# Kernel tuning notes

Hardware: AMD Instinct MI355X
Metric: run time of the kernel (lower is better)

Reference implementation:

```python
import jax, jax.numpy as jnp
import numpy as np
from jax import lax

B, C, H, W = 32, 684, 16, 64
HID, A, CK, K = 256, 512, 512, 11


def setup_inputs() -> dict:
    key = jax.random.key(0)
    ks = jax.random.split(key, 12)
    s = 0.02
    return {
        "cnn_features": jax.random.normal(ks[0], (B, C, H, W), jnp.float32),
        "hidden": jax.random.normal(ks[1], (B, HID), jnp.float32),
        "alpha_sum": jax.random.uniform(ks[2], (B, 1, H, W), jnp.float32),
        "image_mask": jnp.ones((B, 1, H, W), jnp.float32),
        # hidden_weight: Linear(HID -> A)
        "Wh": jax.random.normal(ks[3], (A, HID), jnp.float32) * s,
        "bh": jnp.zeros((A,), jnp.float32),
        # encoder_feature_conv: Conv2d(C -> A, 1x1) == pointwise linear
        "Wec": jax.random.normal(ks[4], (A, C), jnp.float32) * s,
        "bec": jnp.zeros((A,), jnp.float32),
        # attention_conv: Conv2d(1 -> CK, 11x11, pad 5, no bias)
        "Wac": jax.random.normal(ks[5], (CK, 1, K, K), jnp.float32) * s,
        # attention_weight: Linear(CK -> A, no bias)
        "Waw": jax.random.normal(ks[6], (A, CK), jnp.float32) * s,
        # alpha_convert: Linear(A -> 1)
        "Wv": jax.random.normal(ks[7], (1, A), jnp.float32) * s,
        "bv": jnp.zeros((1,), jnp.float32),
    }


def reference(cnn_features, hidden, alpha_sum, image_mask,
              Wh, bh, Wec, bec, Wac, Waw, Wv, bv):
    # query = hidden_weight(hidden): [B, A]
    query = hidden @ Wh.T + bh
    # attention_conv(alpha_sum): [B, CK, H, W]
    ast = lax.conv_general_dilated(
        alpha_sum, Wac, window_strides=(1, 1),
        padding=[(K // 2, K // 2), (K // 2, K // 2)],
        dimension_numbers=("NCHW", "OIHW", "NCHW"))
    # attention_weight on permuted conv output: [B, H, W, A]
    coverage_alpha = jnp.einsum("bkhw,ak->bhwa", ast, Waw)
    # encoder_feature_conv (1x1 conv == pointwise linear): [B, H, W, A]
    cnn_trans = jnp.einsum("bchw,ac->bhwa", cnn_features, Wec) + bec
    # additive attention score
    alpha_score = jnp.tanh(query[:, None, None, :] + coverage_alpha + cnn_trans)
    # alpha_convert -> scalar energy per position: [B, H, W]
    energy = jnp.einsum("bhwa,a->bhw", alpha_score, Wv[0]) + bv[0]
    energy = energy - energy.max()  # global max-subtract as in original
    energy_exp = jnp.exp(energy) * image_mask[:, 0]
    denom = energy_exp.sum(axis=(-1, -2))[:, None, None] + 1e-10
    alpha = energy_exp / denom  # [B, H, W]
    alpha_sum_new = alpha[:, None, :, :] + alpha_sum  # [B, 1, H, W]
    # context: weighted spatial sum over features -> [B, C]
    context_vector = jnp.einsum("bhw,bchw->bc", alpha, cnn_features)
    return (context_vector, alpha, alpha_sum_new)
```

## Files before the change

kernel.cpp:

```cpp
#include <hip/hip_runtime.h>
#include <hip/hip_bf16.h>
#include <math.h>

#define Bn   32
#define Cn   684
#define Hn   16
#define Wn   64
#define HWn  1024
#define HIDn 256
#define An   512
#define KKn  121
#define CREAL 805
#define CPAD 832
#define NSTEP 26
#define NBLK 256

#define OUT_ALPHA 21888
#define OUT_ASUM  (21888 + 32768)

typedef short short8 __attribute__((ext_vector_type(8)));
typedef float floatx4 __attribute__((ext_vector_type(4)));

__device__ __forceinline__ unsigned short f2bf(float f) {
    union { float f; unsigned int i; } v; v.f = f;
    unsigned int i = v.i;
    return (unsigned short)((i + 0x7fffu + ((i >> 16) & 1u)) >> 16);
}
__device__ __forceinline__ unsigned int cvt2(float lo, float hi) {
    __hip_bfloat162 h = __float22bfloat162_rn(float2{lo, hi});
    union { __hip_bfloat162 h; unsigned int u; } cv; cv.h = h;
    return cv.u;
}

__device__ __forceinline__ size_t bfr_idx(int n, int k) {
    return ((((size_t)(n >> 4) * 26 + (k >> 5)) * 64
             + ((k >> 3) & 3) * 16 + (n & 15)) * 8) + (k & 7);
}

__global__ __launch_bounds__(256) void k_prep(
    const float* __restrict__ hidden,
    const float* __restrict__ Wh,
    const float* __restrict__ bh,
    const float* __restrict__ bec,
    const float* __restrict__ Wec,
    const float* __restrict__ Wac,
    const float* __restrict__ Waw,
    float* __restrict__ query,
    unsigned short* __restrict__ Bfr)
{
    __shared__ float sbuf[512];
    const int blk = blockIdx.x, t = threadIdx.x;
    if (blk < 512) {
        const int a = blk;
        sbuf[t]       = Waw[(size_t)a * 512 + t];
        sbuf[t + 256] = Waw[(size_t)a * 512 + t + 256];
        __syncthreads();
        for (int cp = t; cp < Cn; cp += 256)
            Bfr[bfr_idx(a, cp)] = f2bf(Wec[(size_t)a * Cn + cp]);
        if (t < KKn) {
            float s = 0.f;
            #pragma unroll 8
            for (int k = 0; k < 512; ++k)
                s = fmaf(sbuf[k], Wac[k * KKn + t], s);
            Bfr[bfr_idx(a, Cn + t)] = f2bf(s);
        }
        for (int cp = CREAL + t; cp < CPAD; cp += 256)
            Bfr[bfr_idx(a, cp)] = 0;
    } else {
        const int b = blk - 512;
        sbuf[t] = (t < HIDn) ? hidden[b * HIDn + t] : 0.f;
        __syncthreads();
        for (int a = t; a < An; a += 256) {
            const float4* wp = (const float4*)(Wh + (size_t)a * HIDn);
            float s = bh[a] + bec[a];
            #pragma unroll 8
            for (int i = 0; i < HIDn / 4; ++i) {
                float4 w = wp[i];
                s = fmaf(sbuf[4 * i],     w.x, s);
                s = fmaf(sbuf[4 * i + 1], w.y, s);
                s = fmaf(sbuf[4 * i + 2], w.z, s);
                s = fmaf(sbuf[4 * i + 3], w.w, s);
            }
            query[b * An + a] = s;
        }
    }
}

__device__ __forceinline__ float fetchU(const float* __restrict__ X,
                                        const float* plane,
                                        int m, int row) {
    if (row < Cn)   return X[(size_t)row * HWn + m];
    if (row < CREAL) {
        int ij = row - Cn; int di = ij / 11, dj = ij - di * 11;
        return plane[di * 74 + m + dj];
    }
    return 0.f;
}

__global__ __launch_bounds__(256, 4) void k_energy(
    const float* __restrict__ X,
    const float* __restrict__ asum,
    const float* __restrict__ Wv,
    const float* __restrict__ query,
    const unsigned short* __restrict__ Bfr,
    float* __restrict__ energy)
{
    __shared__ __align__(16) unsigned short As[2][64 * 40];
    __shared__ float plane[11 * 74 + 2];
    __shared__ float qs[NBLK];
    __shared__ float wvs[NBLK];
    __shared__ float red[4][64];

    const int t = threadIdx.x;
    const int d = blockIdx.x;
    const int nh  = (d >> 3) & 1;
    const int pid = (d >> 4) * 8 + (d & 7);
    const int hh = pid & 15, b = pid >> 4;
    const int w = t >> 6, lane = t & 63;
    const int q = lane >> 4, r = lane & 15;
    const int nbase = nh * NBLK;
    const int mA = t & 63;
    const int koA = t >> 6;

    const float* Xb = X + (size_t)b * Cn * HWn + hh * Wn;
    const unsigned short* Bp = Bfr + (size_t)(nh * 16 + w * 4) * 26 * 512;

    for (int i = t; i < 11 * 74; i += 256) {
        int di = i / 74, cc = i - di * 74;
        int h2 = hh + di - 5, w2 = cc - 5;
        float v = 0.f;
        if (h2 >= 0 && h2 < Hn && w2 >= 0 && w2 < Wn)
            v = asum[b * HWn + h2 * Wn + w2];
        plane[i] = v;
    }
    qs[t]  = query[b * An + nbase + t];
    wvs[t] = Wv[nbase + t];
    {
        const float* xp = Xb + (size_t)(koA * 8) * HWn + mA;
        uint4 u;
        u.x = cvt2(xp[0],              xp[(size_t)1 * HWn]);
        u.y = cvt2(xp[(size_t)2 * HWn], xp[(size_t)3 * HWn]);
        u.z = cvt2(xp[(size_t)4 * HWn], xp[(size_t)5 * HWn]);
        u.w = cvt2(xp[(size_t)6 * HWn], xp[(size_t)7 * HWn]);
        *(uint4*)&As[0][mA * 40 + koA * 8] = u;
    }
    __syncthreads();

    floatx4 acc[4][4];
    #pragma unroll
    for (int mf = 0; mf < 4; ++mf)
        #pragma unroll
        for (int nf = 0; nf < 4; ++nf)
            acc[mf][nf] = (floatx4){0.f, 0.f, 0.f, 0.f};

    for (int ch = 0; ch < NSTEP; ++ch) {
        const int cur = ch & 1;

        short8 bf[4];
        #pragma unroll
        for (int nf = 0; nf < 4; ++nf)
            bf[nf] = *(const short8*)(Bp + ((size_t)(nf * 26 + ch)) * 512 + lane * 8);

        short8 af[4];
        #pragma unroll
        for (int mf = 0; mf < 4; ++mf)
            af[mf] = *(const short8*)&As[cur][(mf * 16 + r) * 40 + q * 8];

        if (ch < NSTEP - 1) {
            const int c0 = (ch + 1) * 32 + koA * 8;
            float va[8];
            if (c0 + 7 < Cn) {
                const float* xp = Xb + (size_t)c0 * HWn + mA;
                #pragma unroll
                for (int j = 0; j < 8; ++j)
                    va[j] = xp[(size_t)j * HWn];
            } else {
                #pragma unroll
                for (int j = 0; j < 8; ++j)
                    va[j] = fetchU(Xb, plane, mA, c0 + j);
            }
            uint4 u;
            u.x = cvt2(va[0], va[1]);
            u.y = cvt2(va[2], va[3]);
            u.z = cvt2(va[4], va[5]);
            u.w = cvt2(va[6], va[7]);
            *(uint4*)&As[cur ^ 1][mA * 40 + koA * 8] = u;
        }

        #pragma unroll
        for (int mf = 0; mf < 4; ++mf)
            #pragma unroll
            for (int nf = 0; nf < 4; ++nf)
                acc[mf][nf] = __builtin_amdgcn_mfma_f32_16x16x32_bf16(
                    af[mf], bf[nf], acc[mf][nf], 0, 0, 0);

        __syncthreads();
    }

    float ep[16];
    #pragma unroll
    for (int i = 0; i < 16; ++i) ep[i] = 0.f;
    #pragma unroll
    for (int nf = 0; nf < 4; ++nf) {
        int nl = w * 64 + nf * 16 + r;
        float qv = qs[nl], wv = wvs[nl];
        #pragma unroll
        for (int mf = 0; mf < 4; ++mf)
            #pragma unroll
            for (int rg = 0; rg < 4; ++rg) {
                float x = acc[mf][nf][rg] + qv;
                float e2 = __expf(2.f * x);
                float th = 1.f - 2.f * __builtin_amdgcn_rcpf(e2 + 1.f);
                ep[mf * 4 + rg] += wv * th;
            }
    }
    #pragma unroll
    for (int i = 0; i < 16; ++i) {
        #pragma unroll
        for (int msk = 1; msk <= 8; msk <<= 1)
            ep[i] += __shfl_xor(ep[i], msk, 64);
    }
    if (r == 0) {
        #pragma unroll
        for (int mf = 0; mf < 4; ++mf)
            #pragma unroll
            for (int rg = 0; rg < 4; ++rg)
                red[w][mf * 16 + q * 4 + rg] = ep[mf * 4 + rg];
    }
    __syncthreads();
    if (t < 64) {
        float s = red[0][t] + red[1][t] + red[2][t] + red[3][t];
        atomicAdd(&energy[b * HWn + hh * Wn + t], s);
    }
}

__global__ __launch_bounds__(256) void k_softmax(
    const float* __restrict__ mask,
    const float* __restrict__ asum,
    float* __restrict__ energy,
    float* __restrict__ out)
{
    __shared__ float rsm[8];
    const int b = blockIdx.x;
    const int t = threadIdx.x, lane = t & 63, wid = t >> 6;

    float e[4], ex[4];
    #pragma unroll
    for (int i = 0; i < 4; ++i) e[i] = energy[b * HWn + i * 256 + t];
    float m = fmaxf(fmaxf(e[0], e[1]), fmaxf(e[2], e[3]));
    for (int off = 32; off >= 1; off >>= 1) m = fmaxf(m, __shfl_down(m, off, 64));
    if (lane == 0) rsm[wid] = m;
    __syncthreads();
    if (t == 0)
        rsm[4] = fmaxf(fmaxf(rsm[0], rsm[1]), fmaxf(rsm[2], rsm[3]));
    __syncthreads();
    const float M = rsm[4];
    float s = 0.f;
    #pragma unroll
    for (int i = 0; i < 4; ++i) {
        ex[i] = expf(e[i] - M) * mask[b * HWn + i * 256 + t];
        s += ex[i];
    }
    for (int off = 32; off >= 1; off >>= 1) s += __shfl_down(s, off, 64);
    __syncthreads();
    if (lane == 0) rsm[wid] = s;
    __syncthreads();
    if (t == 0) rsm[5] = rsm[0] + rsm[1] + rsm[2] + rsm[3] + 1e-10f;
    __syncthreads();
    const float denom = rsm[5];
    #pragma unroll
    for (int i = 0; i < 4; ++i) {
        int p = i * 256 + t;
        float a = ex[i] / denom;
        energy[b * HWn + p] = a;
        out[OUT_ALPHA + b * HWn + p] = a;
        out[OUT_ASUM  + b * HWn + p] = a + asum[b * HWn + p];
    }
}

__global__ __launch_bounds__(256) void k_ctx(
    const float* __restrict__ X,
    const float* __restrict__ alpha,
    float* __restrict__ out)
{
    __shared__ float al[1024];
    const int bx = blockIdx.x, b = blockIdx.y;
    const int t = threadIdx.x, lane = t & 63, wid = t >> 6;

    #pragma unroll
    for (int i = 0; i < 4; ++i) al[i * 256 + t] = alpha[b * HWn + i * 256 + t];
    __syncthreads();

    const int c = bx * 4 + wid;
    const float* xp = X + ((size_t)(b * Cn + c)) * HWn;
    float s2 = 0.f;
    #pragma unroll
    for (int i = 0; i < 4; ++i) {
        int off = i * 256 + lane * 4;
        float4 x = *(const float4*)(xp + off);
        float4 a = *(const float4*)(al + off);
        s2 = fmaf(a.x, x.x, s2);
        s2 = fmaf(a.y, x.y, s2);
        s2 = fmaf(a.z, x.z, s2);
        s2 = fmaf(a.w, x.w, s2);
    }
    for (int off = 32; off >= 1; off >>= 1) s2 += __shfl_down(s2, off, 64);
    if (lane == 0) out[b * Cn + c] = s2;
}

extern "C" void kernel_launch(void* const* d_in, const int* in_sizes, int n_in,
                              void* d_out, int out_size, void* d_ws, size_t ws_size,
                              hipStream_t stream)
{
    const float* X      = (const float*)d_in[0];
    const float* hidden = (const float*)d_in[1];
    const float* asum   = (const float*)d_in[2];
    const float* mask   = (const float*)d_in[3];
    const float* Wh     = (const float*)d_in[4];
    const float* bh     = (const float*)d_in[5];
    const float* Wec    = (const float*)d_in[6];
    const float* bec    = (const float*)d_in[7];
    const float* Wac    = (const float*)d_in[8];
    const float* Waw    = (const float*)d_in[9];
    const float* Wv     = (const float*)d_in[10];
    (void)in_sizes; (void)n_in; (void)out_size; (void)ws_size;

    float* out = (float*)d_out;
    float* ws = (float*)d_ws;
    float* query  = ws;
    float* energy = ws + 16384;
    unsigned short* Bfr = (unsigned short*)(ws + 16384 + 32768);

    hipMemsetAsync(energy, 0, HWn * Bn * sizeof(float), stream);
    k_prep    <<<dim3(544),      dim3(256), 0, stream>>>(hidden, Wh, bh, bec,
                                                         Wec, Wac, Waw, query, Bfr);
    k_energy  <<<dim3(1024),     dim3(256), 0, stream>>>(X, asum, Wv, query, Bfr, energy);
    k_softmax <<<dim3(32),       dim3(256), 0, stream>>>(mask, asum, energy, out);
    k_ctx     <<<dim3(171, 32),  dim3(256), 0, stream>>>(X, energy, out);
}
```

Measured before the change: 262.2 us.

## Double energy-kernel threads to 512, shrink per-warp N tile, fuse energy memset into prep

After: 238.3 us. 9.1% less time.

```diff
diff --git a/kernel.cpp b/kernel.cpp
--- a/kernel.cpp
+++ b/kernel.cpp
@@ -46,7 +46,8 @@
     const float* __restrict__ Wac,
     const float* __restrict__ Waw,
     float* __restrict__ query,
-    unsigned short* __restrict__ Bfr)
+    unsigned short* __restrict__ Bfr,
+    float* __restrict__ energy)
 {
     __shared__ float sbuf[512];
     const int blk = blockIdx.x, t = threadIdx.x;
@@ -66,7 +67,7 @@
         }
         for (int cp = CREAL + t; cp < CPAD; cp += 256)
             Bfr[bfr_idx(a, cp)] = 0;
-    } else {
+    } else if (blk < 544) {
         const int b = blk - 512;
         sbuf[t] = (t < HIDn) ? hidden[b * HIDn + t] : 0.f;
         __syncthreads();
@@ -83,21 +84,15 @@
             }
             query[b * An + a] = s;
         }
-    }
-}
-
-__device__ __forceinline__ float fetchU(const float* __restrict__ X,
-                                        const float* plane,
-                                        int m, int row) {
-    if (row < Cn)   return X[(size_t)row * HWn + m];
-    if (row < CREAL) {
-        int ij = row - Cn; int di = ij / 11, dj = ij - di * 11;
-        return plane[di * 74 + m + dj];
-    }
-    return 0.f;
-}
-
-__global__ __launch_bounds__(256, 4) void k_energy(
+    } else {
+        const int b = blk - 544;
+        #pragma unroll
+        for (int i = 0; i < 4; ++i)
+            energy[b * HWn + i * 256 + t] = 0.f;
+    }
+}
+
+__global__ __launch_bounds__(512, 4) void k_energy(
     const float* __restrict__ X,
     const float* __restrict__ asum,
     const float* __restrict__ Wv,
@@ -106,10 +101,11 @@
     float* __restrict__ energy)
 {
     __shared__ __align__(16) unsigned short As[2][64 * 40];
-    __shared__ float plane[11 * 74 + 2];
+    __shared__ float plane[878];
+    __shared__ int   lut[148];
     __shared__ float qs[NBLK];
     __shared__ float wvs[NBLK];
-    __shared__ float red[4][64];
+    __shared__ float red[8][64];
 
     const int t = threadIdx.x;
     const int d = blockIdx.x;
@@ -119,46 +115,53 @@
     const int w = t >> 6, lane = t & 63;
     const int q = lane >> 4, r = lane & 15;
     const int nbase = nh * NBLK;
-    const int mA = t & 63;
-    const int koA = t >> 6;
+    const int mA = lane;
 
     const float* Xb = X + (size_t)b * Cn * HWn + hh * Wn;
-    const unsigned short* Bp = Bfr + (size_t)(nh * 16 + w * 4) * 26 * 512;
-
-    for (int i = t; i < 11 * 74; i += 256) {
-        int di = i / 74, cc = i - di * 74;
-        int h2 = hh + di - 5, w2 = cc - 5;
+    const unsigned short* Bp = Bfr + (size_t)(nh * 16 + w * 2) * 26 * 512;
+
+    for (int i = t; i < 878; i += 512) {
         float v = 0.f;
-        if (h2 >= 0 && h2 < Hn && w2 >= 0 && w2 < Wn)
-            v = asum[b * HWn + h2 * Wn + w2];
+        if (i < 814) {
+            int di = i / 74, cc = i - di * 74;
+            int h2 = hh + di - 5, w2 = cc - 5;
+            if (h2 >= 0 && h2 < Hn && w2 >= 0 && w2 < Wn)
+                v = asum[b * HWn + h2 * Wn + w2];
+        }
         plane[i] = v;
     }
-    qs[t]  = query[b * An + nbase + t];
-    wvs[t] = Wv[nbase + t];
+    if (t < 148) {
+        int off = 814;
+        if (t < 121) { int di = t / 11; off = di * 74 + (t - di * 11); }
+        lut[t] = off;
+    }
+    if (t < NBLK) {
+        qs[t]  = query[b * An + nbase + t];
+        wvs[t] = Wv[nbase + t];
+    }
     {
-        const float* xp = Xb + (size_t)(koA * 8) * HWn + mA;
-        uint4 u;
-        u.x = cvt2(xp[0],              xp[(size_t)1 * HWn]);
-        u.y = cvt2(xp[(size_t)2 * HWn], xp[(size_t)3 * HWn]);
-        u.z = cvt2(xp[(size_t)4 * HWn], xp[(size_t)5 * HWn]);
-        u.w = cvt2(xp[(size_t)6 * HWn], xp[(size_t)7 * HWn]);
-        *(uint4*)&As[0][mA * 40 + koA * 8] = u;
-    }
-    __syncthreads();
-
-    floatx4 acc[4][4];
+        const float* xp = Xb + (size_t)(w * 4) * HWn + mA;
+        float v0 = xp[0];
+        float v1 = xp[(size_t)1 * HWn];
+        float v2 = xp[(size_t)2 * HWn];
+        float v3 = xp[(size_t)3 * HWn];
+        *(uint2*)&As[0][mA * 40 + w * 4] = make_uint2(cvt2(v0, v1), cvt2(v2, v3));
+    }
+    __syncthreads();
+
+    floatx4 acc[4][2];
     #pragma unroll
     for (int mf = 0; mf < 4; ++mf)
         #pragma unroll
-        for (int nf = 0; nf < 4; ++nf)
+        for (int nf = 0; nf < 2; ++nf)
             acc[mf][nf] = (floatx4){0.f, 0.f, 0.f, 0.f};
 
     for (int ch = 0; ch < NSTEP; ++ch) {
         const int cur = ch & 1;
 
-        short8 bf[4];
-        #pragma unroll
-        for (int nf = 0; nf < 4; ++nf)
+        short8 bf[2];
+        #pragma unroll
+        for (int nf = 0; nf < 2; ++nf)
             bf[nf] = *(const short8*)(Bp + ((size_t)(nf * 26 + ch)) * 512 + lane * 8);
 
         short8 af[4];
@@ -167,30 +170,22 @@
             af[mf] = *(const short8*)&As[cur][(mf * 16 + r) * 40 + q * 8];
 
         if (ch < NSTEP - 1) {
-            const int c0 = (ch + 1) * 32 + koA * 8;
-            float va[8];
-            if (c0 + 7 < Cn) {
-                const float* xp = Xb + (size_t)c0 * HWn + mA;
-                #pragma unroll
-                for (int j = 0; j < 8; ++j)
-                    va[j] = xp[(size_t)j * HWn];
-            } else {
-                #pragma unroll
-                for (int j = 0; j < 8; ++j)
-                    va[j] = fetchU(Xb, plane, mA, c0 + j);
+            const int c0 = (ch + 1) * 32 + w * 4;
+            float va[4];
+            #pragma unroll
+            for (int j = 0; j < 4; ++j) {
+                const int row = c0 + j;
+                if (row < Cn) va[j] = Xb[(size_t)row * HWn + mA];
+                else          va[j] = plane[lut[row - Cn] + mA];
             }
-            uint4 u;
-            u.x = cvt2(va[0], va[1]);
-            u.y = cvt2(va[2], va[3]);
-            u.z = cvt2(va[4], va[5]);
-            u.w = cvt2(va[6], va[7]);
-            *(uint4*)&As[cur ^ 1][mA * 40 + koA * 8] = u;
+            *(uint2*)&As[cur ^ 1][mA * 40 + w * 4] =
+                make_uint2(cvt2(va[0], va[1]), cvt2(va[2], va[3]));
         }
 
         #pragma unroll
         for (int mf = 0; mf < 4; ++mf)
             #pragma unroll
-            for (int nf = 0; nf < 4; ++nf)
+            for (int nf = 0; nf < 2; ++nf)
                 acc[mf][nf] = __builtin_amdgcn_mfma_f32_16x16x32_bf16(
                     af[mf], bf[nf], acc[mf][nf], 0, 0, 0);
 
@@ -201,8 +196,8 @@
     #pragma unroll
     for (int i = 0; i < 16; ++i) ep[i] = 0.f;
     #pragma unroll
-    for (int nf = 0; nf < 4; ++nf) {
-        int nl = w * 64 + nf * 16 + r;
+    for (int nf = 0; nf < 2; ++nf) {
+        int nl = w * 32 + nf * 16 + r;
         float qv = qs[nl], wv = wvs[nl];
         #pragma unroll
         for (int mf = 0; mf < 4; ++mf)
@@ -229,7 +224,9 @@
     }
     __syncthreads();
     if (t < 64) {
-        float s = red[0][t] + red[1][t] + red[2][t] + red[3][t];
+        float s = 0.f;
+        #pragma unroll
+        for (int ww = 0; ww < 8; ++ww) s += red[ww][t];
         atomicAdd(&energy[b * HWn + hh * Wn + t], s);
     }
 }
@@ -331,10 +328,9 @@
     float* energy = ws + 16384;
     unsigned short* Bfr = (unsigned short*)(ws + 16384 + 32768);
 
-    hipMemsetAsync(energy, 0, HWn * Bn * sizeof(float), stream);
-    k_prep    <<<dim3(544),      dim3(256), 0, stream>>>(hidden, Wh, bh, bec,
-                                                         Wec, Wac, Waw, query, Bfr);
-    k_energy  <<<dim3(1024),     dim3(256), 0, stream>>>(X, asum, Wv, query, Bfr, energy);
+    k_prep    <<<dim3(576),      dim3(256), 0, stream>>>(hidden, Wh, bh, bec,
+                                                         Wec, Wac, Waw, query, Bfr, energy);
+    k_energy  <<<dim3(1024),     dim3(512), 0, stream>>>(X, asum, Wv, query, Bfr, energy);
     k_softmax <<<dim3(32),       dim3(256), 0, stream>>>(mask, asum, energy, out);
     k_ctx     <<<dim3(171, 32),  dim3(256), 0, stream>>>(X, energy, out);
 }
```
